# Performance work log

Measured on AMD Instinct MI355X. Metric: run time of the kernel, lower is better.

## Reference

```python
import jax, jax.numpy as jnp
import numpy as np

N, E, DIN, DH, DOUT, G = 100000, 1600000, 128, 128, 40, 512


def setup_inputs() -> dict:
    key = jax.random.key(0)
    ks = jax.random.split(key, 8)
    x = jax.random.normal(ks[0], (N, DIN), dtype=jnp.float32)
    src = jax.random.randint(ks[1], (E,), 0, N)
    dst = jax.random.randint(ks[2], (E,), 0, N)
    batch = jnp.sort(jax.random.randint(ks[3], (N,), 0, G))
    W1 = jax.random.normal(ks[4], (DIN, DH), dtype=jnp.float32) * (1.0 / np.sqrt(DIN))
    b1 = jnp.zeros((DH,), dtype=jnp.float32)
    W2 = jax.random.normal(ks[5], (DH, DOUT), dtype=jnp.float32) * (1.0 / np.sqrt(DH))
    b2 = jnp.zeros((DOUT,), dtype=jnp.float32)
    return {"x": x, "src": src, "dst": dst, "batch": batch,
            "W1": W1, "b1": b1, "W2": W2, "b2": b2, "num_graphs": G}


def gcn_conv(h, src, dst, n, W, b):
    # PyG GCNConv: linear transform, then D^-1/2 (A + I) D^-1/2 aggregation.
    h = h @ W  # [n, d_out]
    # degree on destination nodes, including self-loop weight 1
    deg = jax.ops.segment_sum(jnp.ones_like(dst, dtype=h.dtype), dst, num_segments=n) + 1.0
    dinv = jax.lax.rsqrt(deg)  # deg >= 1 so always finite
    coef = dinv[src] * dinv[dst]  # [E]
    agg = jax.ops.segment_sum(h[src] * coef[:, None], dst, num_segments=n)
    agg = agg + h * (dinv * dinv)[:, None]  # self-loop term
    return agg + b


def reference(x, src, dst, batch, W1, b1, W2, b2, num_graphs):
    n = x.shape[0]
    h = jax.nn.relu(gcn_conv(x, src, dst, n, W1, b1))  # dropout = identity (eval mode)
    h = jax.nn.relu(gcn_conv(h, src, dst, n, W2, b2))
    # global mean pool over graphs in the batch
    cnt = jax.ops.segment_sum(jnp.ones((n,), dtype=h.dtype), batch, num_segments=num_graphs)
    pooled = jax.ops.segment_sum(h, batch, num_segments=num_graphs) / jnp.maximum(cnt, 1.0)[:, None]
    return jax.nn.log_softmax(pooled, axis=1)
```

## Files before the change

kernel.cpp:

```cpp
#include <hip/hip_runtime.h>
#include <math.h>


typedef __attribute__((ext_vector_type(4))) float f32x4;
typedef __attribute__((ext_vector_type(2))) float f32x2;
typedef __attribute__((ext_vector_type(8))) short bf16x8;
typedef __attribute__((ext_vector_type(4))) uint uint4v;
typedef __attribute__((ext_vector_type(2))) uint uint2v;

constexpr int PAD = 64;
constexpr int CAP = 1536;
constexpr int NBMAX = 1600;

static __device__ __forceinline__ ushort f2bf(float f) {
    union { float f; uint u; } v{f};
    uint r = (v.u + 0x7FFF + ((v.u >> 16) & 1)) >> 16;
    return (ushort)r;
}
static __device__ __forceinline__ uint packbf(float lo, float hi) {
    return ((uint)f2bf(hi) << 16) | (uint)f2bf(lo);
}

__global__ __launch_bounds__(1024) void k_binhist(
    const int* __restrict__ src, const int* __restrict__ dst, int E, int nbkt,
    int* __restrict__ cur2, int* __restrict__ bins,
    const float* __restrict__ W1, const float* __restrict__ W2,
    ushort* __restrict__ w1t, ushort* __restrict__ w2t, int histB) {
    __shared__ int lc[NBMAX];
    const int bid = blockIdx.x;
    const int t = threadIdx.x;
    if (bid >= histB) {
        int i = (bid - histB) * 1024 + t;
        if (i < 128 * 128) {
            int n = i >> 7, k = i & 127;
            w1t[i] = f2bf(W1[k * 128 + n]);
        } else if (i < 128 * 128 + 64 * 128) {
            int j = i - 128 * 128;
            int n = j >> 7, k = j & 127;
            w2t[j] = (n < 40) ? f2bf(W2[k * 40 + n]) : (ushort)0;
        }
        return;
    }
    for (int b = t; b < nbkt; b += 1024) lc[b] = 0;
    __syncthreads();
    const int elo = (int)(((long long)E * bid) / histB);
    const int ehi = (int)(((long long)E * (bid + 1)) / histB);
    for (int e = elo + t; e < ehi; e += 1024) {
        int d = __builtin_nontemporal_load(&dst[e]);
        atomicAdd(&lc[d >> 6], 1);
    }
    __syncthreads();
    for (int b = t; b < nbkt; b += 1024) {
        int c = lc[b];
        lc[b] = (c > 0) ? atomicAdd(&cur2[b], c) : 0;
    }
    __syncthreads();
    for (int e = elo + t; e < ehi; e += 1024) {
        int d = __builtin_nontemporal_load(&dst[e]);
        int s = __builtin_nontemporal_load(&src[e]);
        int b = d >> 6;
        int pos = atomicAdd(&lc[b], 1);
        if (pos < CAP) bins[(size_t)b * CAP + pos] = ((d & 63) << 17) | s;
    }
}

__global__ __launch_bounds__(256) void k_fillb(const int* __restrict__ cur2,
                                               const int* __restrict__ bins,
                                               int* __restrict__ degi,
                                               int* __restrict__ colidx, int N) {
    __shared__ int lcnt[64];
    const int b = blockIdx.x;
    const int base = b << 6;
    const int t = threadIdx.x;
    if (t < 64) lcnt[t] = 0;
    __syncthreads();
    int cnt = min(cur2[b], CAP);
    for (int i = t; i < cnt; i += 256) {
        int entry = bins[(size_t)b * CAP + i];
        int d = entry >> 17;
        int s = entry & 0x1FFFF;
        int r = atomicAdd(&lcnt[d], 1);
        if (r < PAD) colidx[((base + d) << 6) + r] = s;
    }
    __syncthreads();
    if (t < 64 && base + t < N) degi[base + t] = lcnt[t];
}

__global__ __launch_bounds__(256) void k_gemm1(const float* __restrict__ A,
                                               const ushort* __restrict__ BT,
                                               const int* __restrict__ degi,
                                               uint* __restrict__ g1u, int M) {
    __shared__ ushort As[64][136];
    __shared__ ushort Bs[128][136];
    const int tid = threadIdx.x;
    const int m0 = blockIdx.x * 64;
#pragma unroll
    for (int i = 0; i < 4; i++) {
        int chunk = tid + i * 256;
        int r = chunk >> 4, c8 = chunk & 15;
        float4 v0 = {0.f, 0.f, 0.f, 0.f}, v1 = {0.f, 0.f, 0.f, 0.f};
        if (m0 + r < M) {
            const float* p = &A[(size_t)(m0 + r) * 128 + c8 * 8];
            v0 = *(const float4*)p;
            v1 = *(const float4*)(p + 4);
        }
        ushort o[8];
        o[0] = f2bf(v0.x); o[1] = f2bf(v0.y); o[2] = f2bf(v0.z); o[3] = f2bf(v0.w);
        o[4] = f2bf(v1.x); o[5] = f2bf(v1.y); o[6] = f2bf(v1.z); o[7] = f2bf(v1.w);
        *(float4*)&As[r][c8 * 8] = *(float4*)o;
    }
#pragma unroll
    for (int i = 0; i < 8; i++) {
        int chunk = tid + i * 256;
        int r = chunk >> 4, c = chunk & 15;
        *(float4*)&Bs[r][c * 8] = *(const float4*)&BT[(size_t)r * 128 + c * 8];
    }
    __syncthreads();
    const int wave = tid >> 6, lane = tid & 63;
    const int arow = wave * 16 + (lane & 15);
    const int kgrp = (lane >> 4) * 8;
    f32x4 acc[8];
#pragma unroll
    for (int i = 0; i < 8; i++) acc[i] = (f32x4){0.f, 0.f, 0.f, 0.f};
#pragma unroll
    for (int kk = 0; kk < 4; kk++) {
        bf16x8 a = *(const bf16x8*)&As[arow][kk * 32 + kgrp];
#pragma unroll
        for (int nf = 0; nf < 8; nf++) {
            bf16x8 b = *(const bf16x8*)&Bs[nf * 16 + (lane & 15)][kk * 32 + kgrp];
            acc[nf] = __builtin_amdgcn_mfma_f32_16x16x32_bf16(b, a, acc[nf], 0, 0, 0);
        }
    }
    const int m = m0 + wave * 16 + (lane & 15);
    float dv = (m < M) ? rsqrtf((float)degi[m] + 1.0f) : 0.f;
#pragma unroll
    for (int nf = 0; nf < 8; nf++) {
        uint u = __builtin_amdgcn_cvt_pk_fp8_f32(dv * acc[nf][0], dv * acc[nf][1],
                                                 0, false);
        u = (uint)__builtin_amdgcn_cvt_pk_fp8_f32(dv * acc[nf][2], dv * acc[nf][3],
                                                  (int)u, true);
        if (m < M) g1u[(size_t)m * 32 + nf * 4 + (lane >> 4)] = u;
    }
}

__global__ __launch_bounds__(256) void k_agg1p(const uint* __restrict__ g1u,
                                               const int* __restrict__ degi,
                                               const int* __restrict__ colidx,
                                               const float* __restrict__ bias,
                                               const ushort* __restrict__ w2t,
                                               uint* __restrict__ pu, int N) {
    __shared__ ushort g2t[16][136];
    __shared__ ushort Bs[64][136];
    __shared__ int sidx[4][64];
    const int tid = threadIdx.x;
    const int w = tid >> 6;
    const int lane = tid & 63;
    const int q = lane >> 4;
    const int l16 = lane & 15;
    const uint2v* hu = (const uint2v*)g1u;
    const int tile0 = blockIdx.x * 16;
#pragma unroll
    for (int i = 0; i < 4; i++) {
        int chunk = tid + i * 256;
        int r = chunk >> 4, c = chunk & 15;
        *(float4*)&Bs[r][c * 8] = *(const float4*)&w2t[(size_t)r * 128 + c * 8];
    }
#pragma unroll
    for (int sub = 0; sub < 4; sub++) {
        const int r = w * 4 + sub;
        const int wid = tile0 + r;
        f32x2 a0 = {0.f, 0.f}, a1 = {0.f, 0.f}, a2 = {0.f, 0.f}, a3 = {0.f, 0.f};
        int dg = 0;
        if (wid < N) {
            dg = degi[wid];
            const int cnt = min(dg, PAD);
            const int beg = wid << 6;
            if (lane < cnt) sidx[w][lane] = colidx[beg + lane];
            int i = 0;
            for (; i + 16 <= cnt; i += 16) {
                uint2v v[4];
#pragma unroll
                for (int k = 0; k < 4; k++) {
                    v[k] = hu[(size_t)sidx[w][i + 4 * k + q] * 16 + l16];
                }
#pragma unroll
                for (int k = 0; k < 4; k++) {
                    a0 += __builtin_amdgcn_cvt_pk_f32_fp8(v[k].x, false);
                    a1 += __builtin_amdgcn_cvt_pk_f32_fp8(v[k].x, true);
                    a2 += __builtin_amdgcn_cvt_pk_f32_fp8(v[k].y, false);
                    a3 += __builtin_amdgcn_cvt_pk_f32_fp8(v[k].y, true);
                }
            }
            for (; i + q < cnt; i += 4) {
                uint2v vv = hu[(size_t)sidx[w][i + q] * 16 + l16];
                a0 += __builtin_amdgcn_cvt_pk_f32_fp8(vv.x, false);
                a1 += __builtin_amdgcn_cvt_pk_f32_fp8(vv.x, true);
                a2 += __builtin_amdgcn_cvt_pk_f32_fp8(vv.y, false);
                a3 += __builtin_amdgcn_cvt_pk_f32_fp8(vv.y, true);
            }
        }
        a0.x += __shfl_xor(a0.x, 16); a0.y += __shfl_xor(a0.y, 16);
        a1.x += __shfl_xor(a1.x, 16); a1.y += __shfl_xor(a1.y, 16);
        a2.x += __shfl_xor(a2.x, 16); a2.y += __shfl_xor(a2.y, 16);
        a3.x += __shfl_xor(a3.x, 16); a3.y += __shfl_xor(a3.y, 16);
        a0.x += __shfl_xor(a0.x, 32); a0.y += __shfl_xor(a0.y, 32);
        a1.x += __shfl_xor(a1.x, 32); a1.y += __shfl_xor(a1.y, 32);
        a2.x += __shfl_xor(a2.x, 32); a2.y += __shfl_xor(a2.y, 32);
        a3.x += __shfl_xor(a3.x, 32); a3.y += __shfl_xor(a3.y, 32);
        if (lane < 16) {
            float dn = rsqrtf((float)dg + 1.0f);
            if (wid < N) {
                uint2v sv = hu[(size_t)wid * 16 + l16];
                a0 += __builtin_amdgcn_cvt_pk_f32_fp8(sv.x, false);
                a1 += __builtin_amdgcn_cvt_pk_f32_fp8(sv.x, true);
                a2 += __builtin_amdgcn_cvt_pk_f32_fp8(sv.y, false);
                a3 += __builtin_amdgcn_cvt_pk_f32_fp8(sv.y, true);
            }
            float4 b0 = *(const float4*)&bias[l16 * 8];
            float4 b1v = *(const float4*)&bias[l16 * 8 + 4];
            float r0 = dn * fmaxf(dn * a0.x + b0.x, 0.f);
            float r1 = dn * fmaxf(dn * a0.y + b0.y, 0.f);
            float r2 = dn * fmaxf(dn * a1.x + b0.z, 0.f);
            float r3 = dn * fmaxf(dn * a1.y + b0.w, 0.f);
            float r4 = dn * fmaxf(dn * a2.x + b1v.x, 0.f);
            float r5 = dn * fmaxf(dn * a2.y + b1v.y, 0.f);
            float r6 = dn * fmaxf(dn * a3.x + b1v.z, 0.f);
            float r7 = dn * fmaxf(dn * a3.y + b1v.w, 0.f);
            uint4v o;
            o.x = packbf(r0, r1);
            o.y = packbf(r2, r3);
            o.z = packbf(r4, r5);
            o.w = packbf(r6, r7);
            *(uint4v*)&g2t[r][l16 * 8] = o;
        }
    }
    __syncthreads();
    const int arow = lane & 15;
    const int kgrp = (lane >> 4) * 8;
    f32x4 acc = {0.f, 0.f, 0.f, 0.f};
#pragma unroll
    for (int kk = 0; kk < 4; kk++) {
        bf16x8 a = *(const bf16x8*)&g2t[arow][kk * 32 + kgrp];
        bf16x8 b = *(const bf16x8*)&Bs[w * 16 + (lane & 15)][kk * 32 + kgrp];
        acc = __builtin_amdgcn_mfma_f32_16x16x32_bf16(b, a, acc, 0, 0, 0);
    }
    const int m = tile0 + (lane & 15);
    uint u = __builtin_amdgcn_cvt_pk_fp8_f32(acc[0], acc[1], 0, false);
    u = (uint)__builtin_amdgcn_cvt_pk_fp8_f32(acc[2], acc[3], (int)u, true);
    if (m < N) pu[(size_t)m * 16 + w * 4 + (lane >> 4)] = u;
}

__global__ __launch_bounds__(256) void k_agg40(const uint* __restrict__ pu,
                                               const int* __restrict__ degi,
                                               const int* __restrict__ colidx,
                                               const float* __restrict__ b2,
                                               float* __restrict__ h2a, int N) {
    __shared__ int sidx[4][64];
    const int w = threadIdx.x >> 6;
    const int lane = threadIdx.x & 63;
    const int wid = (blockIdx.x * 256 + threadIdx.x) >> 6;
    if (wid >= N) return;
    const int q = lane >> 4;
    const int l16 = lane & 15;
    const int dg = degi[wid];
    const int cnt = min(dg, PAD);
    const int beg = wid << 6;
    f32x2 a01 = {0.f, 0.f}, a23 = {0.f, 0.f};
    if (lane < cnt) sidx[w][lane] = colidx[beg + lane];
    int i = 0;
    for (; i + 16 <= cnt; i += 16) {
        uint v[4];
#pragma unroll
        for (int k = 0; k < 4; k++) {
            v[k] = pu[(size_t)sidx[w][i + 4 * k + q] * 16 + l16];
        }
#pragma unroll
        for (int k = 0; k < 4; k++) {
            a01 += __builtin_amdgcn_cvt_pk_f32_fp8(v[k], false);
            a23 += __builtin_amdgcn_cvt_pk_f32_fp8(v[k], true);
        }
    }
    for (; i + q < cnt; i += 4) {
        uint vv = pu[(size_t)sidx[w][i + q] * 16 + l16];
        a01 += __builtin_amdgcn_cvt_pk_f32_fp8(vv, false);
        a23 += __builtin_amdgcn_cvt_pk_f32_fp8(vv, true);
    }
    a01.x += __shfl_xor(a01.x, 16); a01.y += __shfl_xor(a01.y, 16);
    a23.x += __shfl_xor(a23.x, 16); a23.y += __shfl_xor(a23.y, 16);
    a01.x += __shfl_xor(a01.x, 32); a01.y += __shfl_xor(a01.y, 32);
    a23.x += __shfl_xor(a23.x, 32); a23.y += __shfl_xor(a23.y, 32);
    if (lane < 16 && l16 < 10) {
        float dn = rsqrtf((float)dg + 1.0f);
        uint sv = pu[(size_t)wid * 16 + l16];
        a01 += __builtin_amdgcn_cvt_pk_f32_fp8(sv, false);
        a23 += __builtin_amdgcn_cvt_pk_f32_fp8(sv, true);
        float4 bb = *(const float4*)&b2[l16 * 4];
        float4 o;
        o.x = fmaxf(dn * a01.x + bb.x, 0.f);
        o.y = fmaxf(dn * a01.y + bb.y, 0.f);
        o.z = fmaxf(dn * a23.x + bb.z, 0.f);
        o.w = fmaxf(dn * a23.y + bb.w, 0.f);
        *(float4*)&h2a[(size_t)wid * 40 + l16 * 4] = o;
    }
}

__global__ __launch_bounds__(256) void k_pool(const float* __restrict__ h2a,
                                              const int* __restrict__ batch, int N,
                                              int DOUT, float* __restrict__ out) {
    int g = blockIdx.x;
    int t = threadIdx.x;
    int lo = 0, hi = N;
    while (lo < hi) {
        int mid = (lo + hi) >> 1;
        if (batch[mid] < g) lo = mid + 1; else hi = mid;
    }
    int start = lo;
    hi = N;
    while (lo < hi) {
        int mid = (lo + hi) >> 1;
        if (batch[mid] <= g) lo = mid + 1; else hi = mid;
    }
    int end = lo;
    int cnt = end - start;
    int c = t & 63, rr = t >> 6;
    float acc = 0.f;
    if (c < DOUT) {
        for (int i = start + rr; i < end; i += 4) acc += h2a[(size_t)i * DOUT + c];
    }
    __shared__ float sm[4][64];
    sm[rr][c] = acc;
    __syncthreads();
    if (t < 64) {
        float v = (c < DOUT)
                      ? (sm[0][c] + sm[1][c] + sm[2][c] + sm[3][c]) / fmaxf((float)cnt, 1.f)
                      : -1e30f;
        float m = v;
#pragma unroll
        for (int o = 32; o; o >>= 1) m = fmaxf(m, __shfl_xor(m, o));
        float ex = (c < DOUT) ? expf(v - m) : 0.f;
        float s = ex;
#pragma unroll
        for (int o = 32; o; o >>= 1) s += __shfl_xor(s, o);
        if (c < DOUT) out[g * DOUT + c] = (v - m) - logf(s);
    }
}

extern "C" void kernel_launch(void* const* d_in, const int* in_sizes, int n_in,
                              void* d_out, int out_size, void* d_ws, size_t ws_size,
                              hipStream_t stream) {
    const float* x = (const float*)d_in[0];
    const int* src = (const int*)d_in[1];
    const int* dst = (const int*)d_in[2];
    const int* batch = (const int*)d_in[3];
    const float* W1 = (const float*)d_in[4];
    const float* b1 = (const float*)d_in[5];
    const float* W2 = (const float*)d_in[6];
    const float* b2 = (const float*)d_in[7];
    float* out = (float*)d_out;

    const int N = in_sizes[3];
    const int E = in_sizes[1];
    const int DOUT = in_sizes[7];
    const int G = out_size / DOUT;
    const int nbkt = (N + 63) >> 6;

    char* ws = (char*)d_ws;
    size_t off = 0;
    auto alloc = [&](size_t bytes) -> char* {
        char* p = ws + off;
        off += (bytes + 255) & ~(size_t)255;
        return p;
    };
    uint* g1u = (uint*)alloc((size_t)N * 128);
    uint* pu = (uint*)alloc((size_t)N * 64);
    int* colidx = (int*)alloc((size_t)N * PAD * 4);
    int* bins = (int*)alloc((size_t)nbkt * CAP * 4);
    ushort* w1t = (ushort*)alloc(128 * 128 * 2);
    ushort* w2t = (ushort*)alloc(64 * 128 * 2);
    int* degi = (int*)alloc((size_t)N * 4);
    float* h2a = (float*)alloc((size_t)N * 40 * 4);
    char* z0 = ws + off;
    int* cur2 = (int*)alloc((size_t)nbkt * 4);
    size_t zlen = (size_t)((ws + off) - z0);

    hipMemsetAsync(z0, 0, zlen, stream);

    const int TB = 256;
    const int histB = 256;
    const int prepB = (128 * 128 + 64 * 128 + 1023) / 1024;
    k_binhist<<<histB + prepB, 1024, 0, stream>>>(src, dst, E, nbkt, cur2, bins,
                                                  W1, W2, w1t, w2t, histB);
    k_fillb<<<nbkt, TB, 0, stream>>>(cur2, bins, degi, colidx, N);
    k_gemm1<<<(N + 63) / 64, TB, 0, stream>>>(x, w1t, degi, g1u, N);
    k_agg1p<<<(N + 15) / 16, TB, 0, stream>>>(g1u, degi, colidx, b1, w2t, pu, N);
    k_agg40<<<(N + 3) / 4, TB, 0, stream>>>(pu, degi, colidx, b2, h2a, N);
    k_pool<<<G, TB, 0, stream>>>(h2a, batch, N, DOUT, out);
}
```

Before: 189.7 us.

## Split fused layer-1 aggregation and W2 projection into separate kernels

Replaces the fused aggregate-then-project kernel with two kernels. One kernel gathers neighbours and writes the bf16 hidden activations to global memory with nontemporal stores. A separate MFMA GEMM then projects them by W2 into fp8, reusing the g1u buffer as output. This drops the per-block staging of W2 and the four-node serial loop per wave, and gives the gather kernel higher occupancy. The cost is an extra kernel launch plus an N×128 bf16 round trip through global memory.

```diff
diff --git a/kernel.cpp b/kernel.cpp
--- a/kernel.cpp
+++ b/kernel.cpp
@@ -143,111 +143,124 @@
     }
 }
 
-__global__ __launch_bounds__(256) void k_agg1p(const uint* __restrict__ g1u,
-                                               const int* __restrict__ degi,
-                                               const int* __restrict__ colidx,
-                                               const float* __restrict__ bias,
-                                               const ushort* __restrict__ w2t,
-                                               uint* __restrict__ pu, int N) {
-    __shared__ ushort g2t[16][136];
-    __shared__ ushort Bs[64][136];
+__global__ __launch_bounds__(256) void k_agg128(const uint* __restrict__ g1u,
+                                                const int* __restrict__ degi,
+                                                const int* __restrict__ colidx,
+                                                const float* __restrict__ bias,
+                                                ushort* __restrict__ hout, int N) {
     __shared__ int sidx[4][64];
-    const int tid = threadIdx.x;
-    const int w = tid >> 6;
-    const int lane = tid & 63;
+    const int w = threadIdx.x >> 6;
+    const int lane = threadIdx.x & 63;
+    const int wid = (blockIdx.x * 256 + threadIdx.x) >> 6;
+    if (wid >= N) return;
     const int q = lane >> 4;
     const int l16 = lane & 15;
     const uint2v* hu = (const uint2v*)g1u;
-    const int tile0 = blockIdx.x * 16;
+    const int dg = degi[wid];
+    const int cnt = min(dg, PAD);
+    const int beg = wid << 6;
+    f32x2 a0 = {0.f, 0.f}, a1 = {0.f, 0.f}, a2 = {0.f, 0.f}, a3 = {0.f, 0.f};
+    if (lane < cnt) sidx[w][lane] = colidx[beg + lane];
+    int i = 0;
+    for (; i + 16 <= cnt; i += 16) {
+        uint2v v[4];
+#pragma unroll
+        for (int k = 0; k < 4; k++) {
+            v[k] = hu[(size_t)sidx[w][i + 4 * k + q] * 16 + l16];
+        }
+#pragma unroll
+        for (int k = 0; k < 4; k++) {
+            a0 += __builtin_amdgcn_cvt_pk_f32_fp8(v[k].x, false);
+            a1 += __builtin_amdgcn_cvt_pk_f32_fp8(v[k].x, true);
+            a2 += __builtin_amdgcn_cvt_pk_f32_fp8(v[k].y, false);
+            a3 += __builtin_amdgcn_cvt_pk_f32_fp8(v[k].y, true);
+        }
+    }
+    for (; i + q < cnt; i += 4) {
+        uint2v vv = hu[(size_t)sidx[w][i + q] * 16 + l16];
+        a0 += __builtin_amdgcn_cvt_pk_f32_fp8(vv.x, false);
+        a1 += __builtin_amdgcn_cvt_pk_f32_fp8(vv.x, true);
+        a2 += __builtin_amdgcn_cvt_pk_f32_fp8(vv.y, false);
+        a3 += __builtin_amdgcn_cvt_pk_f32_fp8(vv.y, true);
+    }
+    a0.x += __shfl_xor(a0.x, 16); a0.y += __shfl_xor(a0.y, 16);
+    a1.x += __shfl_xor(a1.x, 16); a1.y += __shfl_xor(a1.y, 16);
+    a2.x += __shfl_xor(a2.x, 16); a2.y += __shfl_xor(a2.y, 16);
+    a3.x += __shfl_xor(a3.x, 16); a3.y += __shfl_xor(a3.y, 16);
+    a0.x += __shfl_xor(a0.x, 32); a0.y += __shfl_xor(a0.y, 32);
+    a1.x += __shfl_xor(a1.x, 32); a1.y += __shfl_xor(a1.y, 32);
+    a2.x += __shfl_xor(a2.x, 32); a2.y += __shfl_xor(a2.y, 32);
+    a3.x += __shfl_xor(a3.x, 32); a3.y += __shfl_xor(a3.y, 32);
+    if (lane < 16) {
+        float dn = rsqrtf((float)dg + 1.0f);
+        uint2v sv = hu[(size_t)wid * 16 + l16];
+        a0 += __builtin_amdgcn_cvt_pk_f32_fp8(sv.x, false);
+        a1 += __builtin_amdgcn_cvt_pk_f32_fp8(sv.x, true);
+        a2 += __builtin_amdgcn_cvt_pk_f32_fp8(sv.y, false);
+        a3 += __builtin_amdgcn_cvt_pk_f32_fp8(sv.y, true);
+        float4 b0 = *(const float4*)&bias[l16 * 8];
+        float4 b1v = *(const float4*)&bias[l16 * 8 + 4];
+        float r0 = dn * fmaxf(dn * a0.x + b0.x, 0.f);
+        float r1 = dn * fmaxf(dn * a0.y + b0.y, 0.f);
+        float r2 = dn * fmaxf(dn * a1.x + b0.z, 0.f);
+        float r3 = dn * fmaxf(dn * a1.y + b0.w, 0.f);
+        float r4 = dn * fmaxf(dn * a2.x + b1v.x, 0.f);
+        float r5 = dn * fmaxf(dn * a2.y + b1v.y, 0.f);
+        float r6 = dn * fmaxf(dn * a3.x + b1v.z, 0.f);
+        float r7 = dn * fmaxf(dn * a3.y + b1v.w, 0.f);
+        uint4v o;
+        o.x = packbf(r0, r1);
+        o.y = packbf(r2, r3);
+        o.z = packbf(r4, r5);
+        o.w = packbf(r6, r7);
+        __builtin_nontemporal_store(o, &((uint4v*)hout)[(size_t)wid * 16 + l16]);
+    }
+}
+
+__global__ __launch_bounds__(256) void k_gemm_p(const ushort* __restrict__ A,
+                                                const ushort* __restrict__ BT,
+                                                uint* __restrict__ pu, int M) {
+    __shared__ ushort As[64][136];
+    __shared__ ushort Bs[64][136];
+    const int tid = threadIdx.x;
+    const int m0 = blockIdx.x * 64;
 #pragma unroll
     for (int i = 0; i < 4; i++) {
         int chunk = tid + i * 256;
         int r = chunk >> 4, c = chunk & 15;
-        *(float4*)&Bs[r][c * 8] = *(const float4*)&w2t[(size_t)r * 128 + c * 8];
-    }
-#pragma unroll
-    for (int sub = 0; sub < 4; sub++) {
-        const int r = w * 4 + sub;
-        const int wid = tile0 + r;
-        f32x2 a0 = {0.f, 0.f}, a1 = {0.f, 0.f}, a2 = {0.f, 0.f}, a3 = {0.f, 0.f};
-        int dg = 0;
-        if (wid < N) {
-            dg = degi[wid];
-            const int cnt = min(dg, PAD);
-            const int beg = wid << 6;
-            if (lane < cnt) sidx[w][lane] = colidx[beg + lane];
-            int i = 0;
-            for (; i + 16 <= cnt; i += 16) {
-                uint2v v[4];
-#pragma unroll
-                for (int k = 0; k < 4; k++) {
-                    v[k] = hu[(size_t)sidx[w][i + 4 * k + q] * 16 + l16];
-                }
-#pragma unroll
-                for (int k = 0; k < 4; k++) {
-                    a0 += __builtin_amdgcn_cvt_pk_f32_fp8(v[k].x, false);
-                    a1 += __builtin_amdgcn_cvt_pk_f32_fp8(v[k].x, true);
-                    a2 += __builtin_amdgcn_cvt_pk_f32_fp8(v[k].y, false);
-                    a3 += __builtin_amdgcn_cvt_pk_f32_fp8(v[k].y, true);
-                }
-            }
-            for (; i + q < cnt; i += 4) {
-                uint2v vv = hu[(size_t)sidx[w][i + q] * 16 + l16];
-                a0 += __builtin_amdgcn_cvt_pk_f32_fp8(vv.x, false);
-                a1 += __builtin_amdgcn_cvt_pk_f32_fp8(vv.x, true);
-                a2 += __builtin_amdgcn_cvt_pk_f32_fp8(vv.y, false);
-                a3 += __builtin_amdgcn_cvt_pk_f32_fp8(vv.y, true);
-            }
-        }
-        a0.x += __shfl_xor(a0.x, 16); a0.y += __shfl_xor(a0.y, 16);
-        a1.x += __shfl_xor(a1.x, 16); a1.y += __shfl_xor(a1.y, 16);
-        a2.x += __shfl_xor(a2.x, 16); a2.y += __shfl_xor(a2.y, 16);
-        a3.x += __shfl_xor(a3.x, 16); a3.y += __shfl_xor(a3.y, 16);
-        a0.x += __shfl_xor(a0.x, 32); a0.y += __shfl_xor(a0.y, 32);
-        a1.x += __shfl_xor(a1.x, 32); a1.y += __shfl_xor(a1.y, 32);
-        a2.x += __shfl_xor(a2.x, 32); a2.y += __shfl_xor(a2.y, 32);
-        a3.x += __shfl_xor(a3.x, 32); a3.y += __shfl_xor(a3.y, 32);
-        if (lane < 16) {
-            float dn = rsqrtf((float)dg + 1.0f);
-            if (wid < N) {
-                uint2v sv = hu[(size_t)wid * 16 + l16];
-                a0 += __builtin_amdgcn_cvt_pk_f32_fp8(sv.x, false);
-                a1 += __builtin_amdgcn_cvt_pk_f32_fp8(sv.x, true);
-                a2 += __builtin_amdgcn_cvt_pk_f32_fp8(sv.y, false);
-                a3 += __builtin_amdgcn_cvt_pk_f32_fp8(sv.y, true);
-            }
-            float4 b0 = *(const float4*)&bias[l16 * 8];
-            float4 b1v = *(const float4*)&bias[l16 * 8 + 4];
-            float r0 = dn * fmaxf(dn * a0.x + b0.x, 0.f);
-            float r1 = dn * fmaxf(dn * a0.y + b0.y, 0.f);
-            float r2 = dn * fmaxf(dn * a1.x + b0.z, 0.f);
-            float r3 = dn * fmaxf(dn * a1.y + b0.w, 0.f);
-            float r4 = dn * fmaxf(dn * a2.x + b1v.x, 0.f);
-            float r5 = dn * fmaxf(dn * a2.y + b1v.y, 0.f);
-            float r6 = dn * fmaxf(dn * a3.x + b1v.z, 0.f);
-            float r7 = dn * fmaxf(dn * a3.y + b1v.w, 0.f);
-            uint4v o;
-            o.x = packbf(r0, r1);
-            o.y = packbf(r2, r3);
-            o.z = packbf(r4, r5);
-            o.w = packbf(r6, r7);
-            *(uint4v*)&g2t[r][l16 * 8] = o;
-        }
-    }
-    __syncthreads();
-    const int arow = lane & 15;
+        float4 v = {0.f, 0.f, 0.f, 0.f};
+        if (m0 + r < M) v = *(const float4*)&A[((size_t)(m0 + r)) * 128 + c * 8];
+        *(float4*)&As[r][c * 8] = v;
+    }
+#pragma unroll
+    for (int i = 0; i < 4; i++) {
+        int chunk = tid + i * 256;
+        int r = chunk >> 4, c = chunk & 15;
+        *(float4*)&Bs[r][c * 8] = *(const float4*)&BT[(size_t)r * 128 + c * 8];
+    }
+    __syncthreads();
+    const int wave = tid >> 6, lane = tid & 63;
+    const int arow = wave * 16 + (lane & 15);
     const int kgrp = (lane >> 4) * 8;
-    f32x4 acc = {0.f, 0.f, 0.f, 0.f};
+    f32x4 acc[4];
+#pragma unroll
+    for (int i = 0; i < 4; i++) acc[i] = (f32x4){0.f, 0.f, 0.f, 0.f};
 #pragma unroll
     for (int kk = 0; kk < 4; kk++) {
-        bf16x8 a = *(const bf16x8*)&g2t[arow][kk * 32 + kgrp];
-        bf16x8 b = *(const bf16x8*)&Bs[w * 16 + (lane & 15)][kk * 32 + kgrp];
-        acc = __builtin_amdgcn_mfma_f32_16x16x32_bf16(b, a, acc, 0, 0, 0);
-    }
-    const int m = tile0 + (lane & 15);
-    uint u = __builtin_amdgcn_cvt_pk_fp8_f32(acc[0], acc[1], 0, false);
-    u = (uint)__builtin_amdgcn_cvt_pk_fp8_f32(acc[2], acc[3], (int)u, true);
-    if (m < N) pu[(size_t)m * 16 + w * 4 + (lane >> 4)] = u;
+        bf16x8 a = *(const bf16x8*)&As[arow][kk * 32 + kgrp];
+#pragma unroll
+        for (int nf = 0; nf < 4; nf++) {
+            bf16x8 b = *(const bf16x8*)&Bs[nf * 16 + (lane & 15)][kk * 32 + kgrp];
+            acc[nf] = __builtin_amdgcn_mfma_f32_16x16x32_bf16(b, a, acc[nf], 0, 0, 0);
+        }
+    }
+    const int m = m0 + wave * 16 + (lane & 15);
+#pragma unroll
+    for (int nf = 0; nf < 4; nf++) {
+        uint u = __builtin_amdgcn_cvt_pk_fp8_f32(acc[nf][0], acc[nf][1], 0, false);
+        u = (uint)__builtin_amdgcn_cvt_pk_fp8_f32(acc[nf][2], acc[nf][3], (int)u, true);
+        if (m < M) pu[(size_t)m * 16 + nf * 4 + (lane >> 4)] = u;
+    }
 }
 
 __global__ __launch_bounds__(256) void k_agg40(const uint* __restrict__ pu,
@@ -372,7 +385,8 @@
         return p;
     };
     uint* g1u = (uint*)alloc((size_t)N * 128);
-    uint* pu = (uint*)alloc((size_t)N * 64);
+    ushort* g2 = (ushort*)alloc((size_t)N * 128 * 2);
+    uint* pu = g1u;
     int* colidx = (int*)alloc((size_t)N * PAD * 4);
     int* bins = (int*)alloc((size_t)nbkt * CAP * 4);
     ushort* w1t = (ushort*)alloc(128 * 128 * 2);
@@ -392,7 +406,8 @@
                                                   W1, W2, w1t, w2t, histB);
     k_fillb<<<nbkt, TB, 0, stream>>>(cur2, bins, degi, colidx, N);
     k_gemm1<<<(N + 63) / 64, TB, 0, stream>>>(x, w1t, degi, g1u, N);
-    k_agg1p<<<(N + 15) / 16, TB, 0, stream>>>(g1u, degi, colidx, b1, w2t, pu, N);
+    k_agg128<<<(N + 3) / 4, TB, 0, stream>>>(g1u, degi, colidx, b1, g2, N);
+    k_gemm_p<<<(N + 63) / 64, TB, 0, stream>>>(g2, w2t, pu, N);
     k_agg40<<<(N + 3) / 4, TB, 0, stream>>>(pu, degi, colidx, b2, h2a, N);
     k_pool<<<G, TB, 0, stream>>>(h2a, batch, N, DOUT, out);
 }
```

Result: no change. 192.3 us (+1.3%).
